# Optimization experiments

Measured on AMD Instinct MI355X. Metric: run time of the kernel, lower is better.

The kernel has to match this reference:

```python
import jax, jax.numpy as jnp
import numpy as np

D_MODEL = 1024
N_HEADS = 16
HEAD_DIM = D_MODEL // N_HEADS


def setup_inputs() -> dict:
    key = jax.random.key(0)
    ks = jax.random.split(key, 9)
    B, S = 4, 2048
    x = jax.random.normal(ks[0], (B, S, D_MODEL), dtype=jnp.float32)
    # causal mask, broadcastable to (B, H, S, S); mask==0 -> -inf
    mask = jnp.tril(jnp.ones((S, S), dtype=jnp.int32))[None, None, :, :]
    s = 1.0 / np.sqrt(D_MODEL)
    wq = jax.random.normal(ks[1], (D_MODEL, D_MODEL), dtype=jnp.float32) * s
    wk = jax.random.normal(ks[2], (D_MODEL, D_MODEL), dtype=jnp.float32) * s
    wv = jax.random.normal(ks[3], (D_MODEL, D_MODEL), dtype=jnp.float32) * s
    wo = jax.random.normal(ks[4], (D_MODEL, D_MODEL), dtype=jnp.float32) * s
    bq = jnp.zeros((D_MODEL,), jnp.float32)
    bk = jnp.zeros((D_MODEL,), jnp.float32)
    bv = jnp.zeros((D_MODEL,), jnp.float32)
    bo = jnp.zeros((D_MODEL,), jnp.float32)
    return {"x": x, "mask": mask, "wq": wq, "bq": bq, "wk": wk, "bk": bk,
            "wv": wv, "bv": bv, "wo": wo, "bo": bo}


def reference(x, mask, wq, bq, wk, bk, wv, bv, wo, bo):
    B, S, D = x.shape
    H, Hd = N_HEADS, HEAD_DIM
    # torch nn.Linear: y = x @ W^T + b
    q = (jnp.einsum('bsd,ed->bse', x, wq) + bq).reshape(B, S, H, Hd).transpose(0, 2, 1, 3)
    k = (jnp.einsum('bsd,ed->bse', x, wk) + bk).reshape(B, S, H, Hd).transpose(0, 2, 1, 3)
    v = (jnp.einsum('bsd,ed->bse', x, wv) + bv).reshape(B, S, H, Hd).transpose(0, 2, 1, 3)
    scores = jnp.einsum('bhqd,bhkd->bhqk', q, k) / jnp.sqrt(jnp.float32(Hd))
    scores = jnp.where(mask == 0, -jnp.inf, scores)
    attn = jax.nn.softmax(scores, axis=-1)
    out = jnp.einsum('bhqk,bhkd->bhqd', attn, v)  # (B,H,S,Hd)
    out = out.transpose(0, 2, 1, 3).reshape(B, S, D)
    return jnp.einsum('bsd,ed->bse', out, wo) + bo
```

## Files before the change

### kernel.cpp

```cpp
#include <hip/hip_runtime.h>
#include <hip/hip_bf16.h>
#include <math.h>

using bf16x8 = __attribute__((ext_vector_type(8))) __bf16;
using bf16x4 = __attribute__((ext_vector_type(4))) __bf16;
using f32x4  = __attribute__((ext_vector_type(4))) float;
using f32x16 = __attribute__((ext_vector_type(16))) float;
using u32x4  = __attribute__((ext_vector_type(4))) unsigned;

static constexpr int S_ = 2048;
static constexpr float SCALE_L2E = 0.125f * 1.44269504088896340736f;

__device__ __forceinline__ void gload16(const void* g, void* lds) {
    __builtin_amdgcn_global_load_lds((const __attribute__((address_space(1))) void*)g,
                                     (__attribute__((address_space(3))) void*)lds, 16, 0, 0);
}

__device__ __forceinline__ unsigned pk2(float a, float b) {
    unsigned short lo = __builtin_bit_cast(unsigned short, (__bf16)a);
    unsigned short hi = __builtin_bit_cast(unsigned short, (__bf16)b);
    return (unsigned)lo | ((unsigned)hi << 16);
}

__device__ __forceinline__ float exp2_hw(float x) {
    return __builtin_amdgcn_exp2f(x);
}

__global__ void cast_f32_bf16(const float* __restrict__ src, __bf16* __restrict__ dst, int n4) {
    int i = blockIdx.x * blockDim.x + threadIdx.x;
    if (i < n4) {
        float4 v = reinterpret_cast<const float4*>(src)[i];
        bf16x4 o = { (__bf16)v.x, (__bf16)v.y, (__bf16)v.z, (__bf16)v.w };
        reinterpret_cast<bf16x4*>(dst)[i] = o;
    }
}

__global__ void cast_weights(const float* __restrict__ wq, const float* __restrict__ wk,
                             const float* __restrict__ wv, const float* __restrict__ wo,
                             __bf16* __restrict__ wqkv, __bf16* __restrict__ wob) {
    int i = blockIdx.x * blockDim.x + threadIdx.x;
    const int seg = i >> 18, off = i & 262143;
    const float* src = (seg == 0) ? wq : (seg == 1) ? wk : (seg == 2) ? wv : wo;
    __bf16* dst = (seg == 0) ? wqkv : (seg == 1) ? (wqkv + 1048576)
                : (seg == 2) ? (wqkv + 2097152) : wob;
    float4 v = reinterpret_cast<const float4*>(src)[off];
    bf16x4 o = { (__bf16)v.x, (__bf16)v.y, (__bf16)v.z, (__bf16)v.w };
    reinterpret_cast<bf16x4*>(dst)[off] = o;
}

template <int EPI>
__global__ __launch_bounds__(256) void gemm_bt(
    const __bf16* __restrict__ A, const __bf16* __restrict__ Bt,
    const float* __restrict__ b0, const float* __restrict__ b1, const float* __restrict__ b2,
    __bf16* __restrict__ Qo, __bf16* __restrict__ Ko, __bf16* __restrict__ Vo,
    float* __restrict__ Fo, int K) {
    __shared__ __align__(16) __bf16 LDS_[3][2][4096];
    const int t = threadIdx.x, l = t & 63, w = t >> 6;
    const int m0 = blockIdx.y * 128, n0 = blockIdx.x * 128;
    const int wm = (w >> 1) * 64, wn = (w & 1) * 64;
    f32x4 acc[4][4] = {};

    const int row0 = t >> 2, cw0 = t & 3;
    const int gc = cw0 ^ ((row0 >> 1) & 3);
    const __bf16* Ag0 = A + (size_t)(m0 + row0) * K + gc * 8;
    const __bf16* Ag1 = A + (size_t)(m0 + row0 + 64) * K + gc * 8;
    const __bf16* Bg0 = Bt + (size_t)(n0 + row0) * K + gc * 8;
    const __bf16* Bg1 = Bt + (size_t)(n0 + row0 + 64) * K + gc * 8;
    const int wo512 = w * 512;

#define STAGE(buf, k0)                                          \
    do {                                                        \
        gload16(Ag0 + (k0), &LDS_[buf][0][wo512]);              \
        gload16(Ag1 + (k0), &LDS_[buf][0][2048 + wo512]);       \
        gload16(Bg0 + (k0), &LDS_[buf][1][wo512]);              \
        gload16(Bg1 + (k0), &LDS_[buf][1][2048 + wo512]);       \
    } while (0)

    const int nk = K >> 5;
    STAGE(0, 0);
    STAGE(1, 32);
    int rb = 0, sb = 2;
    const int sc = (l >> 4) ^ ((l >> 1) & 3);
    for (int ki = 0; ki < nk; ++ki) {
        if (ki + 2 < nk) {
            STAGE(sb, (ki + 2) << 5);
            asm volatile("s_waitcnt vmcnt(8)" ::: "memory");
        } else if (ki + 1 < nk) {
            asm volatile("s_waitcnt vmcnt(4)" ::: "memory");
        } else {
            asm volatile("s_waitcnt vmcnt(0)" ::: "memory");
        }
        __builtin_amdgcn_s_barrier();
        const char* rdA = (const char*)&LDS_[rb][0][0];
        const char* rdB = (const char*)&LDS_[rb][1][0];
        bf16x8 af[4], bf[4];
#pragma unroll
        for (int i = 0; i < 4; ++i)
            af[i] = *reinterpret_cast<const bf16x8*>(rdA + (wm + i * 16 + (l & 15)) * 64 + sc * 16);
#pragma unroll
        for (int j = 0; j < 4; ++j)
            bf[j] = *reinterpret_cast<const bf16x8*>(rdB + (wn + j * 16 + (l & 15)) * 64 + sc * 16);
#pragma unroll
        for (int i = 0; i < 4; ++i)
#pragma unroll
            for (int j = 0; j < 4; ++j)
                acc[i][j] = __builtin_amdgcn_mfma_f32_16x16x32_bf16(af[i], bf[j], acc[i][j], 0, 0, 0);
        __builtin_amdgcn_s_barrier();
        rb = (rb == 2) ? 0 : rb + 1;
        sb = (sb == 2) ? 0 : sb + 1;
    }
#undef STAGE

    if (EPI == 0) {
        const int cls = n0 >> 10;
        if (cls < 2) {
            const float* bias = (cls == 0) ? b0 : b1;
#pragma unroll
            for (int j = 0; j < 4; ++j) {
                const int e = n0 + wn + j * 16 + (l & 15);
                const int eh = e & 1023;
                const int h = eh >> 6, hd = eh & 63;
                const float bv = bias[eh];
#pragma unroll
                for (int i = 0; i < 4; ++i)
#pragma unroll
                    for (int r = 0; r < 4; ++r) {
                        const int m = m0 + wm + i * 16 + ((l >> 4) << 2) + r;
                        const int b = m >> 11, s = m & 2047;
                        float v = acc[i][j][r] + bv;
                        if (cls == 0) v *= SCALE_L2E;
                        __bf16* dst = (cls == 0) ? Qo : Ko;
                        dst[((size_t)(b * 16 + h) * 2048 + s) * 64 + hd] = (__bf16)v;
                    }
            }
        } else {
            char* Tr = (char*)&LDS_[0][0][0];
#pragma unroll
            for (int j = 0; j < 4; ++j) {
                const int el = wn + j * 16 + (l & 15);
                const float bv = b2[(n0 & 1023) + el];
#pragma unroll
                for (int i = 0; i < 4; ++i) {
                    const int m4 = wm + i * 16 + ((l >> 4) << 2);
                    const int pos0 = (m4 & 112) | ((m4 & 4) << 1) | ((m4 & 8) >> 1);
                    bf16x4 pkv = { (__bf16)(acc[i][j][0] + bv), (__bf16)(acc[i][j][1] + bv),
                                   (__bf16)(acc[i][j][2] + bv), (__bf16)(acc[i][j][3] + bv) };
                    const int byt = el * 256 + ((pos0 * 2) ^ ((el & 7) << 4));
                    *reinterpret_cast<bf16x4*>(Tr + byt) = pkv;
                }
            }
            __syncthreads();
            const int b = m0 >> 11, sblk = m0 & 2047;
#pragma unroll
            for (int rr = 0; rr < 8; ++rr) {
                const int er = w * 32 + rr * 4 + (l >> 4);
                const int c = l & 15;
                const int slot = c ^ (er & 7);
                bf16x8 vv = *reinterpret_cast<const bf16x8*>(Tr + er * 256 + slot * 16);
                const int eg = (n0 & 1023) + er;
                const int h = eg >> 6, hd = eg & 63;
                char* dst = (char*)(Vo + ((size_t)(b * 16 + h) * 64 + hd) * 2048 + sblk) + c * 16;
                *reinterpret_cast<bf16x8*>(dst) = vv;
            }
        }
    } else {
#pragma unroll
        for (int j = 0; j < 4; ++j) {
            const int e = n0 + wn + j * 16 + (l & 15);
            const float bv = b0[e];
#pragma unroll
            for (int i = 0; i < 4; ++i)
#pragma unroll
                for (int r = 0; r < 4; ++r) {
                    const int m = m0 + wm + i * 16 + ((l >> 4) << 2) + r;
                    Fo[(size_t)m * 1024 + e] = acc[i][j][r] + bv;
                }
        }
    }
}

__global__ __launch_bounds__(256, 3) void attn_fwd(
    const __bf16* __restrict__ Qb, const __bf16* __restrict__ Kb,
    const __bf16* __restrict__ VTb, __bf16* __restrict__ Ob) {
    __shared__ __align__(16) __bf16 Ks[3][4096];
    __shared__ __align__(16) __bf16 Vs[3][4096];
    const int t = threadIdx.x, l = t & 63, w = t >> 6;
    const int id = blockIdx.x;
    const int g = id >> 6, gq = g >> 2, gr = g & 3;
    const int qt = (gq == 0) ? (15 - gr) : (gq == 1) ? gr : (gq == 2) ? (11 - gr) : (4 + gr);
    const int bh = id & 63;
    const int b = bh >> 4, hh = bh & 15;
    const int hl = l >> 5, l31 = l & 31;

    const __bf16* Qg = Qb + (size_t)bh * S_ * 64;
    const __bf16* Kg = Kb + (size_t)bh * S_ * 64;
    const __bf16* Vg = VTb + (size_t)bh * 64 * S_;

    const int qs = qt * 128 + w * 32;
    const int qg = qs + l31;

    const int tr = t >> 3, sl = t & 7;
    const int swz = (sl ^ (tr & 7)) * 8;
    const __bf16* Ksrc0 = Kg + (size_t)tr * 64 + swz;
    const __bf16* Ksrc1 = Kg + (size_t)(tr + 32) * 64 + swz;
    const __bf16* Vsrc0 = Vg + (size_t)tr * S_ + swz;
    const __bf16* Vsrc1 = Vg + (size_t)(tr + 32) * S_ + swz;

#define STAGEKV(buf, kt)                                        \
    do {                                                        \
        gload16(Ksrc0 + (size_t)(kt) * 4096, &Ks[buf][t * 8]);  \
        gload16(Ksrc1 + (size_t)(kt) * 4096, &Ks[buf][t * 8 + 2048]); \
        gload16(Vsrc0 + (kt) * 64, &Vs[buf][t * 8]);            \
        gload16(Vsrc1 + (kt) * 64, &Vs[buf][t * 8 + 2048]);     \
    } while (0)

    bf16x8 qf[4];
#pragma unroll
    for (int c = 0; c < 4; ++c)
        qf[c] = *reinterpret_cast<const bf16x8*>(Qg + (size_t)qg * 64 + c * 16 + hl * 8);

    f32x16 o0 = {}, o1 = {};
    f32x16 l_acc = {};

    const int nkt = 2 * qt + 2;
    STAGEKV(0, 0);
    STAGEKV(1, 1);
    int rb = 0;
    for (int kt = 0; kt < nkt; ++kt) {
        if (kt + 2 < nkt) {
            const int sb = (rb == 0) ? 2 : rb - 1;
            STAGEKV(sb, kt + 2);
            asm volatile("s_waitcnt vmcnt(8)" ::: "memory");
        } else if (kt + 1 < nkt) {
            asm volatile("s_waitcnt vmcnt(4)" ::: "memory");
        } else {
            asm volatile("s_waitcnt vmcnt(0)" ::: "memory");
        }
        __builtin_amdgcn_s_barrier();
        const char* kb = (const char*)&Ks[rb][0];
        const char* vb = (const char*)&Vs[rb][0];
        const int ktb = kt * 64;
        if (ktb <= qs + 31) {
            const int xs = (l & 7) << 4;
            f32x16 s0 = {}, s1 = {};
            __builtin_amdgcn_s_setprio(1);
#pragma unroll
            for (int c = 0; c < 4; ++c) {
                bf16x8 kf0 = *reinterpret_cast<const bf16x8*>(kb + l31 * 128 + ((c * 32 + hl * 16) ^ xs));
                s0 = __builtin_amdgcn_mfma_f32_32x32x16_bf16(kf0, qf[c], s0, 0, 0, 0);
            }
#pragma unroll
            for (int c = 0; c < 4; ++c) {
                bf16x8 kf1 = *reinterpret_cast<const bf16x8*>(kb + (32 + l31) * 128 + ((c * 32 + hl * 16) ^ xs));
                s1 = __builtin_amdgcn_mfma_f32_32x32x16_bf16(kf1, qf[c], s1, 0, 0, 0);
            }
            __builtin_amdgcn_s_setprio(0);
            float p0[16], p1[16];
            const bool bnd = (ktb + 63) > qs;
            if (bnd) {
#pragma unroll
                for (int rr = 0; rr < 16; ++rr) {
                    const int kvr = ktb + (rr & 3) + 8 * (rr >> 2) + 4 * hl;
                    p0[rr] = exp2_hw((kvr > qg) ? -INFINITY : s0[rr]);
                    p1[rr] = exp2_hw((kvr + 32 > qg) ? -INFINITY : s1[rr]);
                }
            } else {
#pragma unroll
                for (int rr = 0; rr < 16; ++rr) { p0[rr] = exp2_hw(s0[rr]); p1[rr] = exp2_hw(s1[rr]); }
            }
            u32x4 w0 = { pk2(p0[0], p0[1]), pk2(p0[2], p0[3]), pk2(p0[4], p0[5]), pk2(p0[6], p0[7]) };
            u32x4 w1 = { pk2(p0[8], p0[9]), pk2(p0[10], p0[11]), pk2(p0[12], p0[13]), pk2(p0[14], p0[15]) };
            u32x4 w2 = { pk2(p1[0], p1[1]), pk2(p1[2], p1[3]), pk2(p1[4], p1[5]), pk2(p1[6], p1[7]) };
            u32x4 w3 = { pk2(p1[8], p1[9]), pk2(p1[10], p1[11]), pk2(p1[12], p1[13]), pk2(p1[14], p1[15]) };
            bf16x8 pf0 = __builtin_bit_cast(bf16x8, w0);
            bf16x8 pf1 = __builtin_bit_cast(bf16x8, w1);
            bf16x8 pf2 = __builtin_bit_cast(bf16x8, w2);
            bf16x8 pf3 = __builtin_bit_cast(bf16x8, w3);
            __builtin_amdgcn_s_setprio(1);
#pragma unroll
            for (int a = 0; a < 2; ++a) {
                const int rb2 = (a * 32 + l31) * 128;
                bf16x8 vf0 = *reinterpret_cast<const bf16x8*>(vb + rb2 + ((0 * 32 + hl * 16) ^ xs));
                bf16x8 vf1 = *reinterpret_cast<const bf16x8*>(vb + rb2 + ((1 * 32 + hl * 16) ^ xs));
                bf16x8 vf2 = *reinterpret_cast<const bf16x8*>(vb + rb2 + ((2 * 32 + hl * 16) ^ xs));
                bf16x8 vf3 = *reinterpret_cast<const bf16x8*>(vb + rb2 + ((3 * 32 + hl * 16) ^ xs));
                if (a == 0) {
                    o0 = __builtin_amdgcn_mfma_f32_32x32x16_bf16(vf0, pf0, o0, 0, 0, 0);
                    o0 = __builtin_amdgcn_mfma_f32_32x32x16_bf16(vf1, pf1, o0, 0, 0, 0);
                    o0 = __builtin_amdgcn_mfma_f32_32x32x16_bf16(vf2, pf2, o0, 0, 0, 0);
                    o0 = __builtin_amdgcn_mfma_f32_32x32x16_bf16(vf3, pf3, o0, 0, 0, 0);
                } else {
                    o1 = __builtin_amdgcn_mfma_f32_32x32x16_bf16(vf0, pf0, o1, 0, 0, 0);
                    o1 = __builtin_amdgcn_mfma_f32_32x32x16_bf16(vf1, pf1, o1, 0, 0, 0);
                    o1 = __builtin_amdgcn_mfma_f32_32x32x16_bf16(vf2, pf2, o1, 0, 0, 0);
                    o1 = __builtin_amdgcn_mfma_f32_32x32x16_bf16(vf3, pf3, o1, 0, 0, 0);
                }
            }
            __builtin_amdgcn_s_setprio(0);
#pragma unroll
            for (int rr = 0; rr < 16; ++rr) l_acc[rr] += p0[rr] + p1[rr];
        }
        __builtin_amdgcn_s_barrier();
        rb = (rb == 2) ? 0 : rb + 1;
    }
#undef STAGEKV
    float sm[16];
#pragma unroll
    for (int rr = 0; rr < 16; ++rr) sm[rr] = l_acc[rr];
#pragma unroll
    for (int s2 = 8; s2 > 0; s2 >>= 1)
#pragma unroll
        for (int rr = 0; rr < 8; ++rr) if (rr < s2) sm[rr] += sm[rr + s2];
    const float l_r = sm[0] + __shfl_xor(sm[0], 32);
    const float inv = 1.0f / l_r;
    __bf16* ob = Ob + (size_t)(b * 2048 + qg) * 1024 + hh * 64;
#pragma unroll
    for (int gq2 = 0; gq2 < 4; ++gq2) {
        bf16x4 v0 = { (__bf16)(o0[4 * gq2 + 0] * inv), (__bf16)(o0[4 * gq2 + 1] * inv),
                      (__bf16)(o0[4 * gq2 + 2] * inv), (__bf16)(o0[4 * gq2 + 3] * inv) };
        bf16x4 v1 = { (__bf16)(o1[4 * gq2 + 0] * inv), (__bf16)(o1[4 * gq2 + 1] * inv),
                      (__bf16)(o1[4 * gq2 + 2] * inv), (__bf16)(o1[4 * gq2 + 3] * inv) };
        *reinterpret_cast<bf16x4*>(ob + 8 * gq2 + 4 * hl) = v0;
        *reinterpret_cast<bf16x4*>(ob + 32 + 8 * gq2 + 4 * hl) = v1;
    }
}

extern "C" void kernel_launch(void* const* d_in, const int* in_sizes, int n_in,
                              void* d_out, int out_size, void* d_ws, size_t ws_size,
                              hipStream_t stream) {
    const float* x  = (const float*)d_in[0];
    const float* wq = (const float*)d_in[2];
    const float* bq = (const float*)d_in[3];
    const float* wk = (const float*)d_in[4];
    const float* bk = (const float*)d_in[5];
    const float* wv = (const float*)d_in[6];
    const float* bv = (const float*)d_in[7];
    const float* wo = (const float*)d_in[8];
    const float* bo = (const float*)d_in[9];
    float* out = (float*)d_out;

    char* ws = (char*)d_ws;
    __bf16* xb   = (__bf16*)(ws);
    __bf16* wqkv = (__bf16*)(ws + 16777216);
    __bf16* wob  = (__bf16*)(ws + 23068672);
    __bf16* Qb   = (__bf16*)(ws + 25165824);
    __bf16* Kb   = (__bf16*)(ws + 41943040);
    __bf16* VTb  = (__bf16*)(ws + 58720256);
    __bf16* Ob   = (__bf16*)(ws + 75497472);

    cast_f32_bf16<<<8192, 256, 0, stream>>>(x, xb, 2097152);
    cast_weights<<<4096, 256, 0, stream>>>(wq, wk, wv, wo, wqkv, wob);

    gemm_bt<0><<<dim3(24, 64), 256, 0, stream>>>(xb, wqkv, bq, bk, bv, Qb, Kb, VTb, nullptr, 1024);
    attn_fwd<<<1024, 256, 0, stream>>>(Qb, Kb, VTb, Ob);
    gemm_bt<1><<<dim3(8, 64), 256, 0, stream>>>(Ob, wob, bo, nullptr, nullptr, nullptr, nullptr, nullptr, out, 1024);
}
```

Before: 156.2 us.

## Merge cast kernels, XCD-aware GEMM block mapping, double-buffer attention for occupancy

Merges the activation and weight cast kernels into one launch, removing a kernel launch and its tail. The GEMMs switch to a 1D grid whose block IDs are remapped so each XCD (block id mod 8) handles a contiguous band of row tiles, aiming for better L2 reuse of the A tiles. The attention kernel drops from triple to double buffered K/V tiles and raises its launch-bounds occupancy target from 3 to 4 blocks. This trades prefetch depth for more resident waves per CU.

```diff
diff --git a/kernel.cpp b/kernel.cpp
--- a/kernel.cpp
+++ b/kernel.cpp
@@ -26,23 +26,23 @@
     return __builtin_amdgcn_exp2f(x);
 }
 
-__global__ void cast_f32_bf16(const float* __restrict__ src, __bf16* __restrict__ dst, int n4) {
+__global__ void cast_all(const float* __restrict__ x, const float* __restrict__ wq,
+                         const float* __restrict__ wk, const float* __restrict__ wv,
+                         const float* __restrict__ wo, __bf16* __restrict__ xb,
+                         __bf16* __restrict__ wqkv, __bf16* __restrict__ wob) {
     int i = blockIdx.x * blockDim.x + threadIdx.x;
-    if (i < n4) {
-        float4 v = reinterpret_cast<const float4*>(src)[i];
-        bf16x4 o = { (__bf16)v.x, (__bf16)v.y, (__bf16)v.z, (__bf16)v.w };
-        reinterpret_cast<bf16x4*>(dst)[i] = o;
-    }
-}
-
-__global__ void cast_weights(const float* __restrict__ wq, const float* __restrict__ wk,
-                             const float* __restrict__ wv, const float* __restrict__ wo,
-                             __bf16* __restrict__ wqkv, __bf16* __restrict__ wob) {
-    int i = blockIdx.x * blockDim.x + threadIdx.x;
-    const int seg = i >> 18, off = i & 262143;
-    const float* src = (seg == 0) ? wq : (seg == 1) ? wk : (seg == 2) ? wv : wo;
-    __bf16* dst = (seg == 0) ? wqkv : (seg == 1) ? (wqkv + 1048576)
-                : (seg == 2) ? (wqkv + 2097152) : wob;
+    const float* src;
+    __bf16* dst;
+    int off;
+    if (i < 2097152) {
+        src = x; dst = xb; off = i;
+    } else {
+        const int j = i - 2097152;
+        const int seg = j >> 18; off = j & 262143;
+        src = (seg == 0) ? wq : (seg == 1) ? wk : (seg == 2) ? wv : wo;
+        dst = (seg == 0) ? wqkv : (seg == 1) ? (wqkv + 1048576)
+            : (seg == 2) ? (wqkv + 2097152) : wob;
+    }
     float4 v = reinterpret_cast<const float4*>(src)[off];
     bf16x4 o = { (__bf16)v.x, (__bf16)v.y, (__bf16)v.z, (__bf16)v.w };
     reinterpret_cast<bf16x4*>(dst)[off] = o;
@@ -53,10 +53,12 @@
     const __bf16* __restrict__ A, const __bf16* __restrict__ Bt,
     const float* __restrict__ b0, const float* __restrict__ b1, const float* __restrict__ b2,
     __bf16* __restrict__ Qo, __bf16* __restrict__ Ko, __bf16* __restrict__ Vo,
-    float* __restrict__ Fo, int K) {
+    float* __restrict__ Fo, int K, int nbx) {
     __shared__ __align__(16) __bf16 LDS_[3][2][4096];
     const int t = threadIdx.x, l = t & 63, w = t >> 6;
-    const int m0 = blockIdx.y * 128, n0 = blockIdx.x * 128;
+    const int id = blockIdx.x;
+    const int xcd = id & 7, j = id >> 3;
+    const int m0 = (xcd * 8 + j / nbx) * 128, n0 = (j % nbx) * 128;
     const int wm = (w >> 1) * 64, wn = (w & 1) * 64;
     f32x4 acc[4][4] = {};
 
@@ -98,13 +100,13 @@
         for (int i = 0; i < 4; ++i)
             af[i] = *reinterpret_cast<const bf16x8*>(rdA + (wm + i * 16 + (l & 15)) * 64 + sc * 16);
 #pragma unroll
-        for (int j = 0; j < 4; ++j)
-            bf[j] = *reinterpret_cast<const bf16x8*>(rdB + (wn + j * 16 + (l & 15)) * 64 + sc * 16);
+        for (int jj = 0; jj < 4; ++jj)
+            bf[jj] = *reinterpret_cast<const bf16x8*>(rdB + (wn + jj * 16 + (l & 15)) * 64 + sc * 16);
 #pragma unroll
         for (int i = 0; i < 4; ++i)
 #pragma unroll
-            for (int j = 0; j < 4; ++j)
-                acc[i][j] = __builtin_amdgcn_mfma_f32_16x16x32_bf16(af[i], bf[j], acc[i][j], 0, 0, 0);
+            for (int jj = 0; jj < 4; ++jj)
+                acc[i][jj] = __builtin_amdgcn_mfma_f32_16x16x32_bf16(af[i], bf[jj], acc[i][jj], 0, 0, 0);
         __builtin_amdgcn_s_barrier();
         rb = (rb == 2) ? 0 : rb + 1;
         sb = (sb == 2) ? 0 : sb + 1;
@@ -116,8 +118,8 @@
         if (cls < 2) {
             const float* bias = (cls == 0) ? b0 : b1;
 #pragma unroll
-            for (int j = 0; j < 4; ++j) {
-                const int e = n0 + wn + j * 16 + (l & 15);
+            for (int jj = 0; jj < 4; ++jj) {
+                const int e = n0 + wn + jj * 16 + (l & 15);
                 const int eh = e & 1023;
                 const int h = eh >> 6, hd = eh & 63;
                 const float bv = bias[eh];
@@ -127,7 +129,7 @@
                     for (int r = 0; r < 4; ++r) {
                         const int m = m0 + wm + i * 16 + ((l >> 4) << 2) + r;
                         const int b = m >> 11, s = m & 2047;
-                        float v = acc[i][j][r] + bv;
+                        float v = acc[i][jj][r] + bv;
                         if (cls == 0) v *= SCALE_L2E;
                         __bf16* dst = (cls == 0) ? Qo : Ko;
                         dst[((size_t)(b * 16 + h) * 2048 + s) * 64 + hd] = (__bf16)v;
@@ -136,15 +138,15 @@
         } else {
             char* Tr = (char*)&LDS_[0][0][0];
 #pragma unroll
-            for (int j = 0; j < 4; ++j) {
-                const int el = wn + j * 16 + (l & 15);
+            for (int jj = 0; jj < 4; ++jj) {
+                const int el = wn + jj * 16 + (l & 15);
                 const float bv = b2[(n0 & 1023) + el];
 #pragma unroll
                 for (int i = 0; i < 4; ++i) {
                     const int m4 = wm + i * 16 + ((l >> 4) << 2);
                     const int pos0 = (m4 & 112) | ((m4 & 4) << 1) | ((m4 & 8) >> 1);
-                    bf16x4 pkv = { (__bf16)(acc[i][j][0] + bv), (__bf16)(acc[i][j][1] + bv),
-                                   (__bf16)(acc[i][j][2] + bv), (__bf16)(acc[i][j][3] + bv) };
+                    bf16x4 pkv = { (__bf16)(acc[i][jj][0] + bv), (__bf16)(acc[i][jj][1] + bv),
+                                   (__bf16)(acc[i][jj][2] + bv), (__bf16)(acc[i][jj][3] + bv) };
                     const int byt = el * 256 + ((pos0 * 2) ^ ((el & 7) << 4));
                     *reinterpret_cast<bf16x4*>(Tr + byt) = pkv;
                 }
@@ -165,25 +167,25 @@
         }
     } else {
 #pragma unroll
-        for (int j = 0; j < 4; ++j) {
-            const int e = n0 + wn + j * 16 + (l & 15);
+        for (int jj = 0; jj < 4; ++jj) {
+            const int e = n0 + wn + jj * 16 + (l & 15);
             const float bv = b0[e];
 #pragma unroll
             for (int i = 0; i < 4; ++i)
 #pragma unroll
                 for (int r = 0; r < 4; ++r) {
                     const int m = m0 + wm + i * 16 + ((l >> 4) << 2) + r;
-                    Fo[(size_t)m * 1024 + e] = acc[i][j][r] + bv;
+                    Fo[(size_t)m * 1024 + e] = acc[i][jj][r] + bv;
                 }
         }
     }
 }
 
-__global__ __launch_bounds__(256, 3) void attn_fwd(
+__global__ __launch_bounds__(256, 4) void attn_fwd(
     const __bf16* __restrict__ Qb, const __bf16* __restrict__ Kb,
     const __bf16* __restrict__ VTb, __bf16* __restrict__ Ob) {
-    __shared__ __align__(16) __bf16 Ks[3][4096];
-    __shared__ __align__(16) __bf16 Vs[3][4096];
+    __shared__ __align__(16) __bf16 Ks[2][4096];
+    __shared__ __align__(16) __bf16 Vs[2][4096];
     const int t = threadIdx.x, l = t & 63, w = t >> 6;
     const int id = blockIdx.x;
     const int g = id >> 6, gq = g >> 2, gr = g & 3;
@@ -224,21 +226,17 @@
 
     const int nkt = 2 * qt + 2;
     STAGEKV(0, 0);
-    STAGEKV(1, 1);
-    int rb = 0;
+    int cur = 0;
     for (int kt = 0; kt < nkt; ++kt) {
-        if (kt + 2 < nkt) {
-            const int sb = (rb == 0) ? 2 : rb - 1;
-            STAGEKV(sb, kt + 2);
-            asm volatile("s_waitcnt vmcnt(8)" ::: "memory");
-        } else if (kt + 1 < nkt) {
+        if (kt + 1 < nkt) {
+            STAGEKV(cur ^ 1, kt + 1);
             asm volatile("s_waitcnt vmcnt(4)" ::: "memory");
         } else {
             asm volatile("s_waitcnt vmcnt(0)" ::: "memory");
         }
         __builtin_amdgcn_s_barrier();
-        const char* kb = (const char*)&Ks[rb][0];
-        const char* vb = (const char*)&Vs[rb][0];
+        const char* kb = (const char*)&Ks[cur][0];
+        const char* vb = (const char*)&Vs[cur][0];
         const int ktb = kt * 64;
         if (ktb <= qs + 31) {
             const int xs = (l & 7) << 4;
@@ -301,7 +299,7 @@
             for (int rr = 0; rr < 16; ++rr) l_acc[rr] += p0[rr] + p1[rr];
         }
         __builtin_amdgcn_s_barrier();
-        rb = (rb == 2) ? 0 : rb + 1;
+        cur ^= 1;
     }
 #undef STAGEKV
     float sm[16];
@@ -348,10 +346,9 @@
     __bf16* VTb  = (__bf16*)(ws + 58720256);
     __bf16* Ob   = (__bf16*)(ws + 75497472);
 
-    cast_f32_bf16<<<8192, 256, 0, stream>>>(x, xb, 2097152);
-    cast_weights<<<4096, 256, 0, stream>>>(wq, wk, wv, wo, wqkv, wob);
-
-    gemm_bt<0><<<dim3(24, 64), 256, 0, stream>>>(xb, wqkv, bq, bk, bv, Qb, Kb, VTb, nullptr, 1024);
+    cast_all<<<12288, 256, 0, stream>>>(x, wq, wk, wv, wo, xb, wqkv, wob);
+
+    gemm_bt<0><<<1536, 256, 0, stream>>>(xb, wqkv, bq, bk, bv, Qb, Kb, VTb, nullptr, 1024, 24);
     attn_fwd<<<1024, 256, 0, stream>>>(Qb, Kb, VTb, Ob);
-    gemm_bt<1><<<dim3(8, 64), 256, 0, stream>>>(Ob, wob, bo, nullptr, nullptr, nullptr, nullptr, nullptr, out, 1024);
-}
+    gemm_bt<1><<<512, 256, 0, stream>>>(Ob, wob, bo, nullptr, nullptr, nullptr, nullptr, nullptr, out, 1024, 8);
+}
```

Result: slower. 176.3 us (+12.9%).
